# Kernel tuning notes

Measured on AMD Instinct MI355X. Metric: run time of the kernel, lower is better.

Reference implementation:

```python
import jax, jax.numpy as jnp
import numpy as np
from jax import lax

DIM = 128
HEADS = 4
B, H, W = 8, 128, 128


def conv1x1(x, w, b):
    # x: [B,C,H,W], w: [O,I,1,1]
    y = lax.conv_general_dilated(x, w, (1, 1), 'VALID',
                                 dimension_numbers=('NCHW', 'OIHW', 'NCHW'))
    return y + b[None, :, None, None]


def dwconv3x3(x, w, b):
    # depthwise: w: [C,1,3,3], groups=C
    C = x.shape[1]
    y = lax.conv_general_dilated(x, w, (1, 1), ((1, 1), (1, 1)),
                                 dimension_numbers=('NCHW', 'OIHW', 'NCHW'),
                                 feature_group_count=C)
    return y + b[None, :, None, None]


def setup_inputs() -> dict:
    key = jax.random.key(0)
    ks = jax.random.split(key, 7)
    s = 0.02
    return {
        'x': jax.random.normal(ks[0], (B, DIM, H, W), jnp.float32),
        'qkv_w': jax.random.normal(ks[1], (3 * DIM, DIM, 1, 1), jnp.float32) * s,
        'qkv_b': jnp.zeros((3 * DIM,), jnp.float32),
        'dw_w': jax.random.normal(ks[2], (3 * DIM, 1, 3, 3), jnp.float32) * s,
        'dw_b': jnp.zeros((3 * DIM,), jnp.float32),
        'proj_w': jax.random.normal(ks[3], (DIM, DIM, 1, 1), jnp.float32) * s,
        'proj_b': jnp.zeros((DIM,), jnp.float32),
        'temperature': jnp.ones((HEADS, 1, 1, 1), jnp.float32),
    }


def reference(x, qkv_w, qkv_b, dw_w, dw_b, proj_w, proj_b, temperature):
    b, C, h, w = x.shape
    heads = temperature.shape[0]
    c = C // heads

    qkv = dwconv3x3(conv1x1(x, qkv_w, qkv_b), dw_w, dw_b)
    q, k, v = jnp.split(qkv, 3, axis=1)

    # b (head c) h w -> b head c h w
    q = q.reshape(b, heads, c, h, w)
    k = k.reshape(b, heads, c, h, w)
    v = v.reshape(b, heads, c, h, w)

    # L2-normalize along H (axis=-2), matching torch F.normalize eps=1e-12
    eps = 1e-12
    q = q / jnp.maximum(jnp.linalg.norm(q, axis=-2, keepdims=True), eps)
    k = k / jnp.maximum(jnp.linalg.norm(k, axis=-2, keepdims=True), eps)

    # attn[b,n,c,j,k] = sum_i q[b,n,c,i,j] * k_[b,n,c,i,k]  -> [b,head,c,W,W]
    attn = jnp.einsum('bncij,bncik->bncjk', q, k) * temperature
    attn = jax.nn.softmax(attn, axis=-2)

    # out[b,n,c,i,k] = sum_j v[b,n,c,i,j] * attn[b,n,c,j,k]
    out = jnp.einsum('bncij,bncjk->bncik', v, attn)
    out = out.reshape(b, C, h, w)
    return conv1x1(out, proj_w, proj_b)
```

## Files before the change

### kernel.cpp

```cpp
#include <hip/hip_runtime.h>

typedef unsigned short u16;
typedef unsigned int   u32;

typedef short bf16x8 __attribute__((ext_vector_type(8)));
typedef float f32x4  __attribute__((ext_vector_type(4)));

__device__ __forceinline__ float bf2f(u16 u) { return __uint_as_float(((u32)u) << 16); }
__device__ __forceinline__ u16 f2bf(float f) {
    u32 u = __float_as_uint(f);
    return (u16)((u + 0x7fffu + ((u >> 16) & 1u)) >> 16);
}

#define MFMA16(a, b, c) __builtin_amdgcn_mfma_f32_16x16x32_bf16(a, b, c, 0, 0, 0)

__global__ __launch_bounds__(256, 4) void k_xpose(const float* __restrict__ x,
                                                  u16* __restrict__ xT) {
    __shared__ u16 Xs[128 * 128];
    const int ptile = blockIdx.x, b = blockIdx.y;
    const int t = threadIdx.x;
    const float* xb = x + (((size_t)b) << 21) + ptile * 128;
#pragma unroll
    for (int i = 0; i < 16; ++i) {
        int idx = i * 256 + t;
        int ci = idx >> 5, pq = idx & 31;
        float4 v = *(const float4*)(xb + (((size_t)ci) << 14) + pq * 4);
        u32 lo = (u32)f2bf(v.x) | ((u32)f2bf(v.y) << 16);
        u32 hi = (u32)f2bf(v.z) | ((u32)f2bf(v.w) << 16);
        uint2 pk; pk.x = lo; pk.y = hi;
        int cq = ci >> 3;
        *(uint2*)(&Xs[ci * 128 + ((pq ^ cq) << 2)]) = pk;
    }
    __syncthreads();
    u16* ob = xT + (((size_t)b) << 21) + ((size_t)(ptile * 128)) * 128;
#pragma unroll
    for (int j = 0; j < 8; ++j) {
        int p = j * 16 + (t >> 4), cq = t & 15;
        u16 tmp[8];
#pragma unroll
        for (int c = 0; c < 8; ++c) {
            int ci = cq * 8 + c;
            tmp[c] = Xs[ci * 128 + (((p >> 2) ^ cq) << 2) + (p & 3)];
        }
        *(uint4*)(&ob[(size_t)p * 128 + cq * 8]) = *(const uint4*)tmp;
    }
}

__global__ __launch_bounds__(512, 2) void k_qkv(const u16* __restrict__ xT,
                                                const float* __restrict__ w,
                                                const float* __restrict__ bias,
                                                u16* __restrict__ out1) {
    extern __shared__ char smem[];
    u16* Bt = (u16*)smem;
    u16* Cs = Bt + 2048 * 8;
    const int h = blockIdx.x, cg = blockIdx.y, b = blockIdx.z;
    const int t = threadIdx.x;

    const u16* xb = xT + (((size_t)b) << 21) + ((size_t)(h * 128)) * 128;
#pragma unroll
    for (int i = 0; i < 4; ++i) {
        int slot = i * 512 + t;
        int p = slot >> 4, g = slot & 15;
        int gg = g ^ (p & 15);
        uint4 v = *(const uint4*)(&xb[p * 128 + gg * 8]);
        *(uint4*)(&Bt[slot * 8]) = v;
    }

    const int wave = t >> 6, lane = t & 63, m16 = lane & 15, quad = lane >> 4;
    bf16x8 afr[4];
    {
        const float* wp0 = w + (size_t)(cg * 128 + wave * 16 + m16) * 128 + quad * 8;
#pragma unroll
        for (int kk = 0; kk < 4; ++kk) {
            float4 w0 = *(const float4*)(wp0 + kk * 32);
            float4 w1 = *(const float4*)(wp0 + kk * 32 + 4);
            bf16x8 a;
            a[0] = (short)f2bf(w0.x); a[1] = (short)f2bf(w0.y);
            a[2] = (short)f2bf(w0.z); a[3] = (short)f2bf(w0.w);
            a[4] = (short)f2bf(w1.x); a[5] = (short)f2bf(w1.y);
            a[6] = (short)f2bf(w1.z); a[7] = (short)f2bf(w1.w);
            afr[kk] = a;
        }
    }
    __syncthreads();

    f32x4 acc[8] = {};
#pragma unroll
    for (int kk = 0; kk < 4; ++kk) {
        const int g = kk * 4 + quad;
#pragma unroll
        for (int nt = 0; nt < 8; ++nt) {
            int p = nt * 16 + m16;
            bf16x8 bf = *(const bf16x8*)(&Bt[p * 128 + ((g ^ (p & 15)) << 3)]);
            acc[nt] = MFMA16(afr[kk], bf, acc[nt]);
        }
    }

    float bv[4];
#pragma unroll
    for (int r = 0; r < 4; ++r) bv[r] = bias[cg * 128 + wave * 16 + quad * 4 + r];
#pragma unroll
    for (int nt = 0; nt < 8; ++nt) {
        int p = nt * 16 + m16;
#pragma unroll
        for (int r = 0; r < 4; ++r)
            Cs[(wave * 16 + quad * 4 + r) * 136 + p] = f2bf(acc[nt][r] + bv[r]);
    }
    __syncthreads();

    u16* ob = out1 + (((size_t)(b * 384 + cg * 128)) << 14) + (h << 7);
#pragma unroll
    for (int it = 0; it < 4; ++it) {
        int idx = it * 512 + t;
        int co = idx >> 4, cp = idx & 15;
        *(uint4*)(&ob[((size_t)co << 14) + cp * 8]) = *(const uint4*)(&Cs[co * 136 + cp * 8]);
    }
}

__global__ __launch_bounds__(256, 4) void k_dw(const u16* __restrict__ in,
                                               const float* __restrict__ w,
                                               const float* __restrict__ bias,
                                               u16* __restrict__ out) {
    __shared__ u16 tile[34 * 144];
    const int htile = blockIdx.x;
    const int ch = blockIdx.y;
    const int b = blockIdx.z;
    const int t = threadIdx.x;
    const u16* base = in + (((size_t)(b * 384 + ch)) << 14);

    if (t < 68) {
        int r = t >> 1, side = t & 1;
        uint4 z = {0, 0, 0, 0};
        *(uint4*)(&tile[r * 144 + side * 136]) = z;
    }
    for (int it = 0; it < 3; ++it) {
        int idx = it * 256 + t;
        if (idx < 544) {
            int r = idx >> 4, cq = idx & 15;
            int y = htile * 32 - 1 + r;
            uint4 v = {0, 0, 0, 0};
            if (y >= 0 && y <= 127) v = *(const uint4*)(base + (y << 7) + cq * 8);
            *(uint4*)(&tile[r * 144 + 8 + cq * 8]) = v;
        }
    }
    float wg[9];
#pragma unroll
    for (int i = 0; i < 9; ++i) wg[i] = w[ch * 9 + i];
    const float bv = bias[ch];
    __syncthreads();

    const int r = t >> 4, cp = t & 15, c0 = cp * 8;
    u16* ob = out + (((size_t)(b * 384 + ch)) << 14) + ((htile * 32) << 7) + c0;
#pragma unroll
    for (int half = 0; half < 2; ++half) {
        const int ro = r + half * 16;
        float acc[8];
#pragma unroll
        for (int c = 0; c < 8; ++c) acc[c] = bv;
#pragma unroll
        for (int dy = 0; dy < 3; ++dy) {
            const u16* row = &tile[(ro + dy) * 144 + 8 + c0];
            float v[10];
            v[0] = bf2f(row[-1]);
            uint4 m = *(const uint4*)row;
            v[1] = bf2f((u16)(m.x & 0xffff)); v[2] = bf2f((u16)(m.x >> 16));
            v[3] = bf2f((u16)(m.y & 0xffff)); v[4] = bf2f((u16)(m.y >> 16));
            v[5] = bf2f((u16)(m.z & 0xffff)); v[6] = bf2f((u16)(m.z >> 16));
            v[7] = bf2f((u16)(m.w & 0xffff)); v[8] = bf2f((u16)(m.w >> 16));
            v[9] = bf2f(row[8]);
#pragma unroll
            for (int dx = 0; dx < 3; ++dx) {
                const float wv = wg[dy * 3 + dx];
#pragma unroll
                for (int c = 0; c < 8; ++c) acc[c] += wv * v[c + dx];
            }
        }
        u32 pk[4];
#pragma unroll
        for (int c2 = 0; c2 < 4; ++c2) {
            u32 lo = f2bf(acc[2 * c2]), hi = f2bf(acc[2 * c2 + 1]);
            pk[c2] = lo | (hi << 16);
        }
        *(uint4*)(ob + (ro << 7)) = *(uint4*)pk;
    }
}

__global__ __launch_bounds__(512, 4) void k_attn(const u16* __restrict__ qkv,
                                                 const float* __restrict__ temp,
                                                 u16* __restrict__ outp) {
    extern __shared__ char smem[];
    u16* Qt = (u16*)smem;
    u16* Kt = Qt + 16384;
    u16* Sg = Qt + 32768;
    float* ps = (float*)(smem + 74752);
    float* rq = (float*)(smem + 76800);
    float* rk = (float*)(smem + 77312);
    u16* Pt = Qt;
    u16* Osh = Kt;

    const int ch = blockIdx.x, b = blockIdx.y;
    const int head = ch >> 5;
    const int t = threadIdx.x;
    const size_t qoff = ((size_t)(b * 384 + ch)) << 14;
    const size_t koff = ((size_t)(b * 384 + 128 + ch)) << 14;
    const size_t voff = ((size_t)(b * 384 + 256 + ch)) << 14;

    const int wave = t >> 6, lane = t & 63, m16 = lane & 15, quad = lane >> 4;

    bf16x8 vfr[4];
    {
        const u16* vrow = qkv + voff + (size_t)(wave * 16 + m16) * 128 + quad * 8;
#pragma unroll
        for (int kk = 0; kk < 4; ++kk)
            vfr[kk] = *(const bf16x8*)(vrow + kk * 32);
    }

    const int ldr = t >> 4, ldj8 = t & 15;
    const size_t ldsrc = (ldr < 16 ? qoff + (size_t)ldr * 128
                                   : koff + (size_t)(ldr - 16) * 128) + ldj8 * 8;
    const int gmat = t >> 8, gig = (t >> 7) & 1, gj = t & 127;
    const u16* gcol = &Sg[(gmat * 16 + gig * 8) * 144 + gj];
    u16* gdstbase = (gmat ? Kt : Qt) + gj * 128;
    float ssq = 0.f;
#pragma unroll
    for (int p = 0; p < 8; ++p) {
        *(uint4*)(&Sg[ldr * 144 + ldj8 * 8]) = *(const uint4*)(&qkv[ldsrc + (size_t)p * 2048]);
        __syncthreads();
        u16 tmp[8];
#pragma unroll
        for (int c = 0; c < 8; ++c) {
            u16 v = gcol[c * 144];
            tmp[c] = v;
            float f = bf2f(v);
            ssq += f * f;
        }
        int g = p * 2 + gig;
        *(uint4*)(gdstbase + ((g ^ (gj & 15)) << 3)) = *(const uint4*)tmp;
        __syncthreads();
    }
    ps[(gmat * 2 + gig) * 128 + gj] = ssq;
    __syncthreads();
    if (t < 256) {
        int mat = t >> 7, j = t & 127;
        float s = ps[(mat * 2) * 128 + j] + ps[(mat * 2 + 1) * 128 + j];
        float r = 1.0f / fmaxf(sqrtf(s), 1e-12f);
        if (mat == 0) rq[j] = r; else rk[j] = r;
    }
    __syncthreads();

    f32x4 S[8] = {};
#pragma unroll
    for (int kk = 0; kk < 4; ++kk) {
        const int sw = ((kk * 4 + quad) ^ m16) << 3;
        bf16x8 bf = *(const bf16x8*)(&Kt[(wave * 16 + m16) * 128 + sw]);
#pragma unroll
        for (int jt = 0; jt < 8; ++jt) {
            bf16x8 af = *(const bf16x8*)(&Qt[(jt * 16 + m16) * 128 + sw]);
            S[jt] = MFMA16(af, bf, S[jt]);
        }
    }

    const float sc = temp[head] * rk[wave * 16 + m16];
    float vals[8][4];
    float vmax = -1e30f;
#pragma unroll
    for (int jt = 0; jt < 8; ++jt)
#pragma unroll
        for (int r = 0; r < 4; ++r) {
            float v = S[jt][r] * (rq[jt * 16 + quad * 4 + r] * sc);
            vals[jt][r] = v;
            vmax = fmaxf(vmax, v);
        }
    vmax = fmaxf(vmax, __shfl_xor(vmax, 16));
    vmax = fmaxf(vmax, __shfl_xor(vmax, 32));
    float sum = 0.f;
#pragma unroll
    for (int jt = 0; jt < 8; ++jt)
#pragma unroll
        for (int r = 0; r < 4; ++r) {
            float e = __expf(vals[jt][r] - vmax);
            vals[jt][r] = e;
            sum += e;
        }
    sum += __shfl_xor(sum, 16);
    sum += __shfl_xor(sum, 32);
    const float inv = 1.0f / sum;

    __syncthreads();

    {
        const int k = wave * 16 + m16;
        u16* prow = Pt + k * 128;
#pragma unroll
        for (int jt = 0; jt < 8; ++jt)
#pragma unroll
            for (int pr = 0; pr < 2; ++pr) {
                int j0 = jt * 16 + quad * 4 + pr * 2;
                u32 pk = (u32)f2bf(vals[jt][pr * 2] * inv) |
                         ((u32)f2bf(vals[jt][pr * 2 + 1] * inv) << 16);
                *(u32*)(prow + (((j0 >> 3) ^ (k & 15)) << 3) + (j0 & 7)) = pk;
            }
    }
    __syncthreads();

    f32x4 O[8] = {};
#pragma unroll
    for (int kk = 0; kk < 4; ++kk) {
        const int sw = ((kk * 4 + quad) ^ m16) << 3;
#pragma unroll
        for (int nt = 0; nt < 8; ++nt) {
            bf16x8 bf = *(const bf16x8*)(&Pt[(nt * 16 + m16) * 128 + sw]);
            O[nt] = MFMA16(vfr[kk], bf, O[nt]);
        }
    }

#pragma unroll
    for (int nt = 0; nt < 8; ++nt) {
        int k = nt * 16 + m16;
#pragma unroll
        for (int r = 0; r < 4; ++r) {
            int i = wave * 16 + quad * 4 + r;
            Osh[i * 128 + (((k >> 3) ^ (i & 15)) << 3) + (k & 7)] = f2bf(O[nt][r]);
        }
    }
    __syncthreads();

    u16* ob = outp + (((size_t)(b * 128 + ch)) << 14);
#pragma unroll
    for (int it = 0; it < 4; ++it) {
        int idx = it * 512 + t;
        int row = idx >> 4, gk = idx & 15;
        uint4 v = *(const uint4*)(&Osh[row * 128 + ((gk ^ (row & 15)) << 3)]);
        *(uint4*)(&ob[(row << 7) + gk * 8]) = v;
    }
}

__global__ __launch_bounds__(512, 1) void k_proj(const u16* __restrict__ ain,
                                                 const float* __restrict__ w,
                                                 const float* __restrict__ bias,
                                                 float* __restrict__ outp) {
    extern __shared__ char smem[];
    u16* xT = (u16*)smem;
    float* Cs = (float*)(xT + 128 * 136);
    const int h = blockIdx.x, b = blockIdx.y;
    const int t = threadIdx.x;

    const u16* ab = ain + (((size_t)(b * 128)) << 14) + (h << 7);
    for (int it = 0; it < 32; ++it) {
        int idx = it * 512 + t;
        int ci = idx >> 7, p = idx & 127;
        xT[p * 136 + ci] = ab[((size_t)ci << 14) + p];
    }
    __syncthreads();

    const int wave = t >> 6, lane = t & 63, m16 = lane & 15, quad = lane >> 4;
    f32x4 acc[8] = {};
    for (int kk = 0; kk < 4; ++kk) {
        const int kb = kk * 32 + quad * 8;
        const float* wp = w + (wave * 16 + m16) * 128 + kb;
        float4 w0 = *(const float4*)wp;
        float4 w1 = *(const float4*)(wp + 4);
        bf16x8 a;
        a[0] = (short)f2bf(w0.x); a[1] = (short)f2bf(w0.y);
        a[2] = (short)f2bf(w0.z); a[3] = (short)f2bf(w0.w);
        a[4] = (short)f2bf(w1.x); a[5] = (short)f2bf(w1.y);
        a[6] = (short)f2bf(w1.z); a[7] = (short)f2bf(w1.w);
#pragma unroll
        for (int nt = 0; nt < 8; ++nt) {
            bf16x8 bf = *(const bf16x8*)(&xT[(nt * 16 + m16) * 136 + kb]);
            acc[nt] = MFMA16(a, bf, acc[nt]);
        }
    }
    float bv[4];
#pragma unroll
    for (int r = 0; r < 4; ++r) bv[r] = bias[wave * 16 + quad * 4 + r];
#pragma unroll
    for (int nt = 0; nt < 8; ++nt) {
        int p = nt * 16 + m16;
#pragma unroll
        for (int r = 0; r < 4; ++r)
            Cs[(wave * 16 + quad * 4 + r) * 132 + p] = acc[nt][r] + bv[r];
    }
    __syncthreads();

    float* ob = outp + (((size_t)(b * 128)) << 14) + (h << 7);
    for (int it = 0; it < 8; ++it) {
        int idx = it * 512 + t;
        int row = idx >> 5, cp = idx & 31;
        *(float4*)(&ob[((size_t)row << 14) + cp * 4]) = *(const float4*)(&Cs[row * 132 + cp * 4]);
    }
}

extern "C" void kernel_launch(void* const* d_in, const int* in_sizes, int n_in,
                              void* d_out, int out_size, void* d_ws, size_t ws_size,
                              hipStream_t stream) {
    const float* x      = (const float*)d_in[0];
    const float* qkv_w  = (const float*)d_in[1];
    const float* qkv_b  = (const float*)d_in[2];
    const float* dw_w   = (const float*)d_in[3];
    const float* dw_b   = (const float*)d_in[4];
    const float* proj_w = (const float*)d_in[5];
    const float* proj_b = (const float*)d_in[6];
    const float* temp   = (const float*)d_in[7];
    float* out = (float*)d_out;

    u16* buf1 = (u16*)d_ws;
    u16* buf2 = buf1 + (size_t)8 * 384 * 16384;

    hipFuncSetAttribute((const void*)k_qkv,  hipFuncAttributeMaxDynamicSharedMemorySize, 67584);
    hipFuncSetAttribute((const void*)k_attn, hipFuncAttributeMaxDynamicSharedMemorySize, 77824);
    hipFuncSetAttribute((const void*)k_proj, hipFuncAttributeMaxDynamicSharedMemorySize, 102400);

    k_xpose<<<dim3(128, 8), 256, 0, stream>>>(x, buf2);
    k_qkv<<<dim3(128, 3, 8), 512, 67584, stream>>>(buf2, qkv_w, qkv_b, buf1);
    k_dw<<<dim3(4, 384, 8), 256, 0, stream>>>(buf1, dw_w, dw_b, buf2);
    k_attn<<<dim3(128, 8), 512, 77824, stream>>>(buf2, temp, buf1);
    k_proj<<<dim3(128, 8), 512, 102400, stream>>>(buf1, proj_w, proj_b, out);
}
```

Baseline: 258.9 us.

## Reuse staged input across all qkv channel groups and restructure proj transpose

The qkv kernel now loops over the three 128-channel output groups inside one block, so each xT tile is loaded into shared memory once instead of three times, at the cost of a third as many blocks doing serial work. The proj kernel replaces its scalar strided transposing load with coalesced 16-byte row loads staged through a small shared buffer and written to a swizzled layout. It also hoists the weight fragments out of the k-loop and writes output directly from registers instead of through a shared staging tile. Shared memory for proj drops sharply and launch bounds are raised to allow more resident blocks, though the direct output stores are less coalesced.

```diff
diff --git a/kernel.cpp b/kernel.cpp
--- a/kernel.cpp
+++ b/kernel.cpp
@@ -46,14 +46,14 @@
     }
 }
 
-__global__ __launch_bounds__(512, 2) void k_qkv(const u16* __restrict__ xT,
+__global__ __launch_bounds__(512, 4) void k_qkv(const u16* __restrict__ xT,
                                                 const float* __restrict__ w,
                                                 const float* __restrict__ bias,
                                                 u16* __restrict__ out1) {
     extern __shared__ char smem[];
     u16* Bt = (u16*)smem;
     u16* Cs = Bt + 2048 * 8;
-    const int h = blockIdx.x, cg = blockIdx.y, b = blockIdx.z;
+    const int h = blockIdx.x, b = blockIdx.y;
     const int t = threadIdx.x;
 
     const u16* xb = xT + (((size_t)b) << 21) + ((size_t)(h * 128)) * 128;
@@ -65,10 +65,12 @@
         uint4 v = *(const uint4*)(&xb[p * 128 + gg * 8]);
         *(uint4*)(&Bt[slot * 8]) = v;
     }
+    __syncthreads();
 
     const int wave = t >> 6, lane = t & 63, m16 = lane & 15, quad = lane >> 4;
-    bf16x8 afr[4];
-    {
+
+    for (int cg = 0; cg < 3; ++cg) {
+        bf16x8 afr[4];
         const float* wp0 = w + (size_t)(cg * 128 + wave * 16 + m16) * 128 + quad * 8;
 #pragma unroll
         for (int kk = 0; kk < 4; ++kk) {
@@ -81,39 +83,40 @@
             a[6] = (short)f2bf(w1.z); a[7] = (short)f2bf(w1.w);
             afr[kk] = a;
         }
-    }
-    __syncthreads();
-
-    f32x4 acc[8] = {};
-#pragma unroll
-    for (int kk = 0; kk < 4; ++kk) {
-        const int g = kk * 4 + quad;
+
+        f32x4 acc[8] = {};
+#pragma unroll
+        for (int kk = 0; kk < 4; ++kk) {
+            const int g = kk * 4 + quad;
+#pragma unroll
+            for (int nt = 0; nt < 8; ++nt) {
+                int p = nt * 16 + m16;
+                bf16x8 bf = *(const bf16x8*)(&Bt[p * 128 + ((g ^ (p & 15)) << 3)]);
+                acc[nt] = MFMA16(afr[kk], bf, acc[nt]);
+            }
+        }
+
+        float bv[4];
+#pragma unroll
+        for (int r = 0; r < 4; ++r) bv[r] = bias[cg * 128 + wave * 16 + quad * 4 + r];
+
+        __syncthreads();
 #pragma unroll
         for (int nt = 0; nt < 8; ++nt) {
             int p = nt * 16 + m16;
-            bf16x8 bf = *(const bf16x8*)(&Bt[p * 128 + ((g ^ (p & 15)) << 3)]);
-            acc[nt] = MFMA16(afr[kk], bf, acc[nt]);
-        }
-    }
-
-    float bv[4];
-#pragma unroll
-    for (int r = 0; r < 4; ++r) bv[r] = bias[cg * 128 + wave * 16 + quad * 4 + r];
-#pragma unroll
-    for (int nt = 0; nt < 8; ++nt) {
-        int p = nt * 16 + m16;
-#pragma unroll
-        for (int r = 0; r < 4; ++r)
-            Cs[(wave * 16 + quad * 4 + r) * 136 + p] = f2bf(acc[nt][r] + bv[r]);
-    }
-    __syncthreads();
-
-    u16* ob = out1 + (((size_t)(b * 384 + cg * 128)) << 14) + (h << 7);
-#pragma unroll
-    for (int it = 0; it < 4; ++it) {
-        int idx = it * 512 + t;
-        int co = idx >> 4, cp = idx & 15;
-        *(uint4*)(&ob[((size_t)co << 14) + cp * 8]) = *(const uint4*)(&Cs[co * 136 + cp * 8]);
+#pragma unroll
+            for (int r = 0; r < 4; ++r)
+                Cs[(wave * 16 + quad * 4 + r) * 136 + p] = f2bf(acc[nt][r] + bv[r]);
+        }
+        __syncthreads();
+
+        u16* ob = out1 + (((size_t)(b * 384 + cg * 128)) << 14) + (h << 7);
+#pragma unroll
+        for (int it = 0; it < 4; ++it) {
+            int idx = it * 512 + t;
+            int co = idx >> 4, cp = idx & 15;
+            *(uint4*)(&ob[((size_t)co << 14) + cp * 8]) = *(const uint4*)(&Cs[co * 136 + cp * 8]);
+        }
     }
 }
 
@@ -335,59 +338,75 @@
     }
 }
 
-__global__ __launch_bounds__(512, 1) void k_proj(const u16* __restrict__ ain,
+__global__ __launch_bounds__(512, 6) void k_proj(const u16* __restrict__ ain,
                                                  const float* __restrict__ w,
                                                  const float* __restrict__ bias,
                                                  float* __restrict__ outp) {
     extern __shared__ char smem[];
-    u16* xT = (u16*)smem;
-    float* Cs = (float*)(xT + 128 * 136);
+    u16* Bt = (u16*)smem;
+    u16* Sg = Bt + 16384;
     const int h = blockIdx.x, b = blockIdx.y;
     const int t = threadIdx.x;
 
-    const u16* ab = ain + (((size_t)(b * 128)) << 14) + (h << 7);
-    for (int it = 0; it < 32; ++it) {
-        int idx = it * 512 + t;
-        int ci = idx >> 7, p = idx & 127;
-        xT[p * 136 + ci] = ab[((size_t)ci << 14) + p];
-    }
-    __syncthreads();
+    const int ldr = t >> 4, ldj8 = t & 15;
+    const int gig = t >> 7, gp = t & 127;
+    const u16* gcol = &Sg[(gig * 8) * 144 + gp];
+    u16* gdst = Bt + gp * 128;
+#pragma unroll
+    for (int ph = 0; ph < 4; ++ph) {
+        int ch = ph * 32 + ldr;
+        *(uint4*)(&Sg[ldr * 144 + ldj8 * 8]) =
+            *(const uint4*)(&ain[(((size_t)(b * 128 + ch)) << 14) + (h << 7) + ldj8 * 8]);
+        __syncthreads();
+        u16 tmp[8];
+#pragma unroll
+        for (int c = 0; c < 8; ++c) tmp[c] = gcol[c * 144];
+        int g = ph * 4 + gig;
+        *(uint4*)(gdst + ((g ^ (gp & 15)) << 3)) = *(const uint4*)tmp;
+        __syncthreads();
+    }
 
     const int wave = t >> 6, lane = t & 63, m16 = lane & 15, quad = lane >> 4;
+    bf16x8 afr[4];
+    {
+        const float* wp0 = w + (size_t)(wave * 16 + m16) * 128 + quad * 8;
+#pragma unroll
+        for (int kk = 0; kk < 4; ++kk) {
+            float4 w0 = *(const float4*)(wp0 + kk * 32);
+            float4 w1 = *(const float4*)(wp0 + kk * 32 + 4);
+            bf16x8 a;
+            a[0] = (short)f2bf(w0.x); a[1] = (short)f2bf(w0.y);
+            a[2] = (short)f2bf(w0.z); a[3] = (short)f2bf(w0.w);
+            a[4] = (short)f2bf(w1.x); a[5] = (short)f2bf(w1.y);
+            a[6] = (short)f2bf(w1.z); a[7] = (short)f2bf(w1.w);
+            afr[kk] = a;
+        }
+    }
+
     f32x4 acc[8] = {};
+#pragma unroll
     for (int kk = 0; kk < 4; ++kk) {
-        const int kb = kk * 32 + quad * 8;
-        const float* wp = w + (wave * 16 + m16) * 128 + kb;
-        float4 w0 = *(const float4*)wp;
-        float4 w1 = *(const float4*)(wp + 4);
-        bf16x8 a;
-        a[0] = (short)f2bf(w0.x); a[1] = (short)f2bf(w0.y);
-        a[2] = (short)f2bf(w0.z); a[3] = (short)f2bf(w0.w);
-        a[4] = (short)f2bf(w1.x); a[5] = (short)f2bf(w1.y);
-        a[6] = (short)f2bf(w1.z); a[7] = (short)f2bf(w1.w);
+        const int g = kk * 4 + quad;
 #pragma unroll
         for (int nt = 0; nt < 8; ++nt) {
-            bf16x8 bf = *(const bf16x8*)(&xT[(nt * 16 + m16) * 136 + kb]);
-            acc[nt] = MFMA16(a, bf, acc[nt]);
-        }
-    }
+            int p = nt * 16 + m16;
+            bf16x8 bf = *(const bf16x8*)(&Bt[p * 128 + ((g ^ (p & 15)) << 3)]);
+            acc[nt] = MFMA16(afr[kk], bf, acc[nt]);
+        }
+    }
+
     float bv[4];
 #pragma unroll
     for (int r = 0; r < 4; ++r) bv[r] = bias[wave * 16 + quad * 4 + r];
+    float* ob = outp + (((size_t)(b * 128)) << 14) + (h << 7);
 #pragma unroll
     for (int nt = 0; nt < 8; ++nt) {
         int p = nt * 16 + m16;
 #pragma unroll
-        for (int r = 0; r < 4; ++r)
-            Cs[(wave * 16 + quad * 4 + r) * 132 + p] = acc[nt][r] + bv[r];
-    }
-    __syncthreads();
-
-    float* ob = outp + (((size_t)(b * 128)) << 14) + (h << 7);
-    for (int it = 0; it < 8; ++it) {
-        int idx = it * 512 + t;
-        int row = idx >> 5, cp = idx & 31;
-        *(float4*)(&ob[((size_t)row << 14) + cp * 4]) = *(const float4*)(&Cs[row * 132 + cp * 4]);
+        for (int r = 0; r < 4; ++r) {
+            int co = wave * 16 + quad * 4 + r;
+            ob[((size_t)co << 14) + p] = acc[nt][r] + bv[r];
+        }
     }
 }
 
@@ -409,11 +428,11 @@
 
     hipFuncSetAttribute((const void*)k_qkv,  hipFuncAttributeMaxDynamicSharedMemorySize, 67584);
     hipFuncSetAttribute((const void*)k_attn, hipFuncAttributeMaxDynamicSharedMemorySize, 77824);
-    hipFuncSetAttribute((const void*)k_proj, hipFuncAttributeMaxDynamicSharedMemorySize, 102400);
+    hipFuncSetAttribute((const void*)k_proj, hipFuncAttributeMaxDynamicSharedMemorySize, 41984);
 
     k_xpose<<<dim3(128, 8), 256, 0, stream>>>(x, buf2);
-    k_qkv<<<dim3(128, 3, 8), 512, 67584, stream>>>(buf2, qkv_w, qkv_b, buf1);
+    k_qkv<<<dim3(128, 8), 512, 67584, stream>>>(buf2, qkv_w, qkv_b, buf1);
     k_dw<<<dim3(4, 384, 8), 256, 0, stream>>>(buf1, dw_w, dw_b, buf2);
     k_attn<<<dim3(128, 8), 512, 77824, stream>>>(buf2, temp, buf1);
-    k_proj<<<dim3(128, 8), 512, 102400, stream>>>(buf1, proj_w, proj_b, out);
-}
+    k_proj<<<dim3(128, 8), 512, 41984, stream>>>(buf1, proj_w, proj_b, out);
+}
```

After: 260.1 us. About the same (+0.5%).
